# Kernel tuning notes

Measured on AMD Instinct MI355X. Metric: run time of the kernel, lower is better.

## Reference

```python
import jax, jax.numpy as jnp
import numpy as np

# Uniform 3-level hierarchy matching HIERALCHY: root has B0 children,
# each of those has B1 children, each of those has B2 leaf children.
B0, B1, B2 = 8, 16, 16
BATCH = 32768


def setup_inputs() -> dict:
    key = jax.random.key(0)
    k0, k1, k2 = jax.random.split(key, 3)
    dc0 = jax.random.uniform(k0, (BATCH, B0), dtype=jnp.float32)
    dc1 = jax.random.uniform(k1, (BATCH, B0 * B1), dtype=jnp.float32)
    dc2 = jax.random.uniform(k2, (BATCH, B0 * B1 * B2), dtype=jnp.float32)
    return {"dc0": dc0, "dc1": dc1, "dc2": dc2}


def reference(dc0, dc1, dc2):
    # Faithful to DET_PROB.one_step: within each sibling group the running
    # probability p_tmp is a CUMULATIVE product across siblings (p_tmp is
    # reassigned inside the loop), and it is carried into the recursion.
    # Hence leaf (a0, a1, a2) gets:
    #   cumprod(dc0)[a0] * cumprod_within_group(dc1)[a0, a1]
    #                    * cumprod_within_group(dc2)[a0*B1 + a1, a2]
    # Leaves are emitted in DFS order == row-major (a0, a1, a2) order.
    B = dc0.shape[0]
    c0 = jnp.cumprod(dc0, axis=1)                          # [B, B0]
    c1 = jnp.cumprod(dc1.reshape(B, B0, B1), axis=2)       # [B, B0, B1]
    c2 = jnp.cumprod(dc2.reshape(B, B0 * B1, B2), axis=2)  # [B, B0*B1, B2]
    prefix = (c0[:, :, None] * c1).reshape(B, B0 * B1, 1)  # [B, B0*B1, 1]
    return (prefix * c2).reshape(B, B0 * B1 * B2)          # [B, 2048]
```

## Files before the change

kernel.cpp:

```cpp
#include <hip/hip_runtime.h>


#define NB0 8
#define NB1 16
#define NB2 16
#define GROUPS (NB0 * NB1)
#define ROW_LEN (GROUPS * NB2)

__global__ __launch_bounds__(512)
void det_prob_kernel(const float* __restrict__ dc0,
                     const float* __restrict__ dc1,
                     const float* __restrict__ dc2,
                     float* __restrict__ out)
{
    const int row = blockIdx.x;
    const int t   = threadIdx.x;

    const size_t row_off = (size_t)row * ROW_LEN;

    const float4 x = reinterpret_cast<const float4*>(dc2 + row_off)[t];

    const int wave = t >> 6;
    const int lane = t & 63;
    const int j    = lane & 3;

    float c0 = 1.0f;
    #pragma unroll
    for (int k = 0; k < NB0; ++k) {
        float v = dc0[(size_t)row * NB0 + k];
        if (k <= wave) c0 *= v;
    }

    float d1 = dc1[(size_t)row * GROUPS + (size_t)wave * NB1 + (lane >> 2)];

    float scan = d1;
    #pragma unroll
    for (int off = 4; off <= 32; off <<= 1) {
        float u = __shfl_up(scan, off, 64);
        if (lane >= off) scan *= u;
    }
    const float prefix = c0 * scan;

    float y0 = x.x;
    float y1 = y0 * x.y;
    float y2 = y1 * x.z;
    float y3 = y2 * x.w;

    const int qbase = lane & ~3;
    const float t0 = __shfl(y3, qbase + 0, 64);
    const float t1 = __shfl(y3, qbase + 1, 64);
    const float t2 = __shfl(y3, qbase + 2, 64);

    float p = prefix;
    if (j > 0) p *= t0;
    if (j > 1) p *= t1;
    if (j > 2) p *= t2;

    float4 o;
    o.x = y0 * p;
    o.y = y1 * p;
    o.z = y2 * p;
    o.w = y3 * p;
    reinterpret_cast<float4*>(out + row_off)[t] = o;
}

extern "C" void kernel_launch(void* const* d_in, const int* in_sizes, int n_in,
                              void* d_out, int out_size, void* d_ws, size_t ws_size,
                              hipStream_t stream) {
    const float* dc0 = (const float*)d_in[0];
    const float* dc1 = (const float*)d_in[1];
    const float* dc2 = (const float*)d_in[2];
    float* out = (float*)d_out;

    const int batch = in_sizes[0] / NB0;
    det_prob_kernel<<<batch, 512, 0, stream>>>(dc0, dc1, dc2, out);
}
```

Before: 430.6 us.

## Use persistent grid-stride blocks with next-row prefetch and nontemporal memory ops

Launches a fixed grid of 4096 blocks that loop over rows with a grid stride instead of one block per row. Each iteration prefetches the next row's dc2 vector and dc1 value before computing the current row, to overlap load latency with compute and stores. Loads of dc2 and stores to out use nontemporal builtins to avoid polluting caches with streaming data. This reduces block launch overhead but relies on fewer resident blocks to saturate memory bandwidth and adds register pressure for the prefetched values.

After: 433.4 us. No clear change (+0.7%).

```diff
diff --git a/kernel.cpp b/kernel.cpp
--- a/kernel.cpp
+++ b/kernel.cpp
@@ -6,62 +6,85 @@
 #define NB2 16
 #define GROUPS (NB0 * NB1)
 #define ROW_LEN (GROUPS * NB2)
+#define GRID 4096
+
+typedef float fx4 __attribute__((ext_vector_type(4)));
 
 __global__ __launch_bounds__(512)
 void det_prob_kernel(const float* __restrict__ dc0,
                      const float* __restrict__ dc1,
                      const float* __restrict__ dc2,
-                     float* __restrict__ out)
+                     float* __restrict__ out,
+                     int batch)
 {
-    const int row = blockIdx.x;
-    const int t   = threadIdx.x;
-
-    const size_t row_off = (size_t)row * ROW_LEN;
-
-    const float4 x = reinterpret_cast<const float4*>(dc2 + row_off)[t];
-
+    const int t    = threadIdx.x;
     const int wave = t >> 6;
     const int lane = t & 63;
     const int j    = lane & 3;
+    const int g    = lane >> 2;
 
-    float c0 = 1.0f;
-    #pragma unroll
-    for (int k = 0; k < NB0; ++k) {
-        float v = dc0[(size_t)row * NB0 + k];
-        if (k <= wave) c0 *= v;
+    const int stride = gridDim.x;
+    int row = blockIdx.x;
+    if (row >= batch) return;
+
+    fx4 x = __builtin_nontemporal_load(
+        reinterpret_cast<const fx4*>(dc2 + (size_t)row * ROW_LEN) + t);
+    float d1 = dc1[(size_t)row * GROUPS + (size_t)wave * NB1 + g];
+
+    while (true) {
+        const int nrow = row + stride;
+
+        fx4   xn  = x;
+        float d1n = d1;
+        if (nrow < batch) {
+            xn = __builtin_nontemporal_load(
+                reinterpret_cast<const fx4*>(dc2 + (size_t)nrow * ROW_LEN) + t);
+            d1n = dc1[(size_t)nrow * GROUPS + (size_t)wave * NB1 + g];
+        }
+
+        float c0 = 1.0f;
+        #pragma unroll
+        for (int k = 0; k < NB0; ++k) {
+            float v = dc0[(size_t)row * NB0 + k];
+            if (k <= wave) c0 *= v;
+        }
+
+        float scan = d1;
+        #pragma unroll
+        for (int off = 4; off <= 32; off <<= 1) {
+            float u = __shfl_up(scan, off, 64);
+            if (lane >= off) scan *= u;
+        }
+        const float prefix = c0 * scan;
+
+        const float y0 = x.x;
+        const float y1 = y0 * x.y;
+        const float y2 = y1 * x.z;
+        const float y3 = y2 * x.w;
+
+        const int qbase = lane & ~3;
+        const float t0 = __shfl(y3, qbase + 0, 64);
+        const float t1 = __shfl(y3, qbase + 1, 64);
+        const float t2 = __shfl(y3, qbase + 2, 64);
+
+        float p = prefix;
+        if (j > 0) p *= t0;
+        if (j > 1) p *= t1;
+        if (j > 2) p *= t2;
+
+        fx4 o;
+        o.x = y0 * p;
+        o.y = y1 * p;
+        o.z = y2 * p;
+        o.w = y3 * p;
+        __builtin_nontemporal_store(
+            o, reinterpret_cast<fx4*>(out + (size_t)row * ROW_LEN) + t);
+
+        if (nrow >= batch) break;
+        row = nrow;
+        x = xn;
+        d1 = d1n;
     }
-
-    float d1 = dc1[(size_t)row * GROUPS + (size_t)wave * NB1 + (lane >> 2)];
-
-    float scan = d1;
-    #pragma unroll
-    for (int off = 4; off <= 32; off <<= 1) {
-        float u = __shfl_up(scan, off, 64);
-        if (lane >= off) scan *= u;
-    }
-    const float prefix = c0 * scan;
-
-    float y0 = x.x;
-    float y1 = y0 * x.y;
-    float y2 = y1 * x.z;
-    float y3 = y2 * x.w;
-
-    const int qbase = lane & ~3;
-    const float t0 = __shfl(y3, qbase + 0, 64);
-    const float t1 = __shfl(y3, qbase + 1, 64);
-    const float t2 = __shfl(y3, qbase + 2, 64);
-
-    float p = prefix;
-    if (j > 0) p *= t0;
-    if (j > 1) p *= t1;
-    if (j > 2) p *= t2;
-
-    float4 o;
-    o.x = y0 * p;
-    o.y = y1 * p;
-    o.z = y2 * p;
-    o.w = y3 * p;
-    reinterpret_cast<float4*>(out + row_off)[t] = o;
 }
 
 extern "C" void kernel_launch(void* const* d_in, const int* in_sizes, int n_in,
@@ -73,5 +96,7 @@
     float* out = (float*)d_out;
 
     const int batch = in_sizes[0] / NB0;
-    det_prob_kernel<<<batch, 512, 0, stream>>>(dc0, dc1, dc2, out);
+    int grid = GRID;
+    if (grid > batch) grid = batch;
+    det_prob_kernel<<<grid, 512, 0, stream>>>(dc0, dc1, dc2, out, batch);
 }
```
